# Performance work log

Measured on AMD Instinct MI355X. Metric: run time of the kernel, lower is better.

Reference implementation:

```python
import jax, jax.numpy as jnp
import numpy as np

D, M, K, L, H, BS = 128, 8, 256, 2, 256, 1024


def setup_inputs() -> dict:
    key = jax.random.key(0)
    ks = jax.random.split(key, 7)
    s_d = 1.0 / np.sqrt(D)
    s_2d = 1.0 / np.sqrt(2 * D)
    s_h = 1.0 / np.sqrt(H)
    x = jax.random.normal(ks[0], (BS, D), jnp.float32)
    codebook0 = jax.random.uniform(ks[1], (K, D), jnp.float32, -s_d, s_d)
    codebooks = jax.random.uniform(ks[2], (M - 1, K, D), jnp.float32, -s_d, s_d)
    Wc = jax.random.uniform(ks[3], (M - 1, D, 2 * D), jnp.float32, -s_2d, s_2d)
    bc = jax.random.uniform(ks[4], (M - 1, D), jnp.float32, -s_2d, s_2d)
    W1 = jax.random.uniform(ks[5], (M - 1, L, H, D), jnp.float32, -s_d, s_d)
    W2 = jax.random.uniform(ks[6], (M - 1, L, D, H), jnp.float32, -s_h, s_h)
    return {"x": x, "codebook0": codebook0, "codebooks": codebooks,
            "Wc": Wc, "bc": bc, "W1": W1, "W2": W2}


def _step_targets(xhat, cb, Wc_m, bc_m, W1_m, W2_m):
    """Candidate quantization targets for one step. xhat:[bs,d], cb:[K,d] -> [bs,K,d].
    MLPconcat(concat(zqs, xhat)) is split into the zqs part and the xhat part so the
    [bs*K, 2d] repeat of the torch code is never materialized (same math)."""
    Wz, Wx = Wc_m[:, :D], Wc_m[:, D:]          # Linear(2d,d): y = cc @ W.T + b
    z = cb[None, :, :] + (cb @ Wz.T)[None, :, :] + (xhat @ Wx.T)[:, None, :] + bc_m  # [bs,K,d]
    for l in range(L):
        z = z + jnp.maximum(jnp.einsum('bkd,hd->bkh', z, W1_m[l]), 0.0) @ W2_m[l].T
    return z + xhat[:, None, :]


def _encode(x, codebook0, codebooks, Wc, bc, W1, W2):
    # step 0: plain nearest-centroid assignment (assign_to_codebook)
    d0 = (x * x).sum(-1, keepdims=True) + (codebook0 * codebook0).sum(-1) - 2.0 * x @ codebook0.T
    code0 = jnp.argmin(d0, axis=1)
    xhat = codebook0[code0]
    codes = [code0]
    xn = (x * x).sum(-1, keepdims=True)        # [bs,1]
    for m in range(M - 1):
        z = _step_targets(xhat, codebooks[m], Wc[m], bc[m], W1[m], W2[m])  # [bs,K,d]
        dist = xn + (z * z).sum(-1) - 2.0 * jnp.einsum('bd,bkd->bk', x, z)
        idx = jnp.argmin(dist, axis=1)
        xhat = jnp.take_along_axis(z, idx[:, None, None], axis=1)[:, 0, :]
        codes.append(idx)
    return jnp.stack(codes, axis=1)            # [bs, M] int


def _decode(codes, codebook0, codebooks, Wc, bc, W1, W2):
    xhat = codebook0[codes[:, 0]]
    side = [xhat]
    for m in range(M - 1):
        zq = codebooks[m][codes[:, m + 1]]     # [bs,d]
        Wz, Wx = Wc[m][:, :D], Wc[m][:, D:]
        z = zq + zq @ Wz.T + xhat @ Wx.T + bc[m]
        for l in range(L):
            z = z + jnp.maximum(z @ W1[m, l].T, 0.0) @ W2[m, l].T
        xhat = xhat + z
        side.append(xhat)
    return xhat, side


def reference(x, codebook0, codebooks, Wc, bc, W1, W2):
    # forward(): encode under no_grad, then differentiable decode with side outputs
    codes = jax.lax.stop_gradient(_encode(x, codebook0, codebooks, Wc, bc, W1, W2))
    xhat, side = _decode(codes, codebook0, codebooks, Wc, bc, W1, W2)
    return (xhat, codes, tuple(side))
```

## Files before the change

kernel.cpp:

```cpp
#include <hip/hip_runtime.h>


typedef _Float16 f16;
typedef f16 half4_t __attribute__((ext_vector_type(4)));
typedef f16 half8_t __attribute__((ext_vector_type(8)));
typedef float f32x16 __attribute__((ext_vector_type(16)));

#define OUT_CODES 131072
#define OUT_SIDE  139264

#define WS_XHAT  0
#define WS_RB    131072
#define WS_Y     262144
#define WS_ZC    393216
#define WS_BESTD 425984
#define WS_BESTI 430080
#define WS_BESTZ 434176
#define WS_WSPLIT 960000
#define NW1 458752

#define HLO 8192

__device__ __forceinline__ f32x16 mfma_f16(half8_t a, half8_t b, f32x16 c) {
  return __builtin_amdgcn_mfma_f32_32x32x16_f16(a, b, c, 0, 0, 0);
}

__global__ __launch_bounds__(256) void k_wsplit(const float* __restrict__ W1,
    const float* __restrict__ W2, f16* __restrict__ wsh)
{
  int i = (blockIdx.x * 256 + threadIdx.x) * 4;
  const float* src;
  f16* hi;
  if (i < NW1) { src = W1 + i; hi = wsh + i; }
  else         { src = W2 + (i - NW1); hi = wsh + 2 * NW1 + (i - NW1); }
  f16* lo = hi + NW1;
  float4 v = *(const float4*)src;
  half4_t h, l;
  float s;
  s = v.x * 256.f; h[0] = (f16)s; l[0] = (f16)(s - (float)h[0]);
  s = v.y * 256.f; h[1] = (f16)s; l[1] = (f16)(s - (float)h[1]);
  s = v.z * 256.f; h[2] = (f16)s; l[2] = (f16)(s - (float)h[2]);
  s = v.w * 256.f; h[3] = (f16)s; l[3] = (f16)(s - (float)h[3]);
  *(half4_t*)hi = h;
  *(half4_t*)lo = l;
}

__global__ __launch_bounds__(256) void k_step0(const float* __restrict__ x,
    const float* __restrict__ cb0, float* __restrict__ ws, float* __restrict__ out)
{
  __shared__ float xs[128];
  __shared__ float redv[4];
  __shared__ int   redi[4];
  __shared__ int   kwin;
  int tx = threadIdx.x, b = blockIdx.x;
  if (tx < 128) xs[tx] = x[b * 128 + tx];
  __syncthreads();
  const float* c = cb0 + tx * 128;
  float s = 0.f;
  for (int d = 0; d < 128; d += 4) {
    float4 cv = *(const float4*)(c + d);
    float4 xv = *(const float4*)(xs + d);
    float a0 = xv.x - cv.x, a1 = xv.y - cv.y, a2 = xv.z - cv.z, a3 = xv.w - cv.w;
    s += a0 * a0 + a1 * a1 + a2 * a2 + a3 * a3;
  }
  float v = s; int idx = tx;
  for (int off = 32; off; off >>= 1) {
    float v2 = __shfl_xor(v, off);
    int   i2 = __shfl_xor(idx, off);
    if (v2 < v || (v2 == v && i2 < idx)) { v = v2; idx = i2; }
  }
  if ((tx & 63) == 0) { redv[tx >> 6] = v; redi[tx >> 6] = idx; }
  __syncthreads();
  if (tx == 0) {
    float bv = redv[0]; int bi = redi[0];
    for (int w = 1; w < 4; w++)
      if (redv[w] < bv || (redv[w] == bv && redi[w] < bi)) { bv = redv[w]; bi = redi[w]; }
    kwin = bi;
    out[OUT_CODES + b * 8] = (float)bi;
  }
  __syncthreads();
  int k = kwin;
  if (tx < 128) {
    float xh = cb0[k * 128 + tx];
    ws[WS_XHAT + b * 128 + tx] = xh;
    ws[WS_RB   + b * 128 + tx] = xs[tx] - xh;
    out[OUT_SIDE + b * 128 + tx] = xh;
  }
}

__global__ __launch_bounds__(128) void k_prep(const float* __restrict__ cb,
    const float* __restrict__ Wc, const float* __restrict__ bcm, float* __restrict__ ws)
{
  __shared__ float row[128];
  int tx = threadIdx.x, blk = blockIdx.x;
  if (blk < 256) {
    row[tx] = cb[blk * 128 + tx];
    __syncthreads();
    const float* wrow = Wc + tx * 256;
    float s = 0.f;
    for (int d = 0; d < 128; d += 4) {
      float4 wv = *(const float4*)(wrow + d);
      float4 zv = *(const float4*)(row + d);
      s += wv.x * zv.x + wv.y * zv.y + wv.z * zv.z + wv.w * zv.w;
    }
    ws[WS_ZC + blk * 128 + tx] = row[tx] + s + bcm[tx];
  } else {
    int b = blk - 256;
    row[tx] = ws[WS_XHAT + b * 128 + tx];
    __syncthreads();
    const float* wrow = Wc + tx * 256 + 128;
    float s = 0.f;
    for (int d = 0; d < 128; d += 4) {
      float4 wv = *(const float4*)(wrow + d);
      float4 zv = *(const float4*)(row + d);
      s += wv.x * zv.x + wv.y * zv.y + wv.z * zv.z + wv.w * zv.w;
    }
    ws[WS_Y + b * 128 + tx] = s;
  }
}

__global__ __launch_bounds__(256, 2) void k_step(const f16* __restrict__ wsh,
    float* __restrict__ ws, int sm)
{
  __shared__ __align__(16) f16 lds[32768];
  f16* Zh = lds;
  f16* Zl = lds + HLO;
  f16* Hh = lds + 2 * HLO;
  f16* Hl = lds + 3 * HLO;
  int tx = threadIdx.x;
  int lane = tx & 63, w = tx >> 6;
  int col = lane & 31, koct = lane >> 5;
  int b = blockIdx.x >> 2, t = blockIdx.x & 3, k0 = t << 6;

  {
    const float* zc = ws + WS_ZC + k0 * 128;
    const float* y  = ws + WS_Y + b * 128;
    for (int idx = tx; idx < 1024; idx += 256) {
      int m = idx & 63, d0 = (idx >> 6) << 3;
      float4 a  = *(const float4*)(zc + m * 128 + d0);
      float4 bb = *(const float4*)(zc + m * 128 + d0 + 4);
      float4 ya = *(const float4*)(y + d0);
      float4 yb = *(const float4*)(y + d0 + 4);
      float sv[8] = {a.x + ya.x, a.y + ya.y, a.z + ya.z, a.w + ya.w,
                     bb.x + yb.x, bb.y + yb.y, bb.z + yb.z, bb.w + yb.w};
      half8_t h8, l8;
#pragma unroll
      for (int j = 0; j < 8; j++) {
        float v = sv[j] * 256.f;
        f16 h = (f16)v; h8[j] = h; l8[j] = (f16)(v - (float)h);
      }
      int c0 = (d0 + ((m & 15) << 3)) & 127;
      *(half8_t*)(Zh + (m << 7) + c0) = h8;
      *(half8_t*)(Zl + (m << 7) + c0) = l8;
    }
  }
  __syncthreads();

  const int rot0 = (col & 15) << 3;
  const f16* Zr0 = Zh + (col << 7);
  const f16* Zr1 = Zh + ((col + 32) << 7);
  const f16* Hr0 = Hh + (col << 7);
  const f16* Hr1 = Hh + ((col + 32) << 7);

  for (int l = 0; l < 2; l++) {
    const f16* w1h = wsh + (size_t)((sm * 2 + l) * 256) * 128;
    const f16* w2h = wsh + 2 * NW1 + (size_t)((sm * 2 + l) * 128) * 256;
    f32x16 acc2[2];
#pragma unroll
    for (int i = 0; i < 16; i++) { acc2[0][i] = 0.f; acc2[1][i] = 0.f; }

    half8_t a1hv[8], a1lv[8];
    {
      const f16* a1p = w1h + (size_t)((w << 5) + col) * 128 + (koct << 3);
#pragma unroll
      for (int kc = 0; kc < 8; kc++) {
        a1hv[kc] = *(const half8_t*)(a1p + (kc << 4));
        a1lv[kc] = *(const half8_t*)(a1p + NW1 + (kc << 4));
      }
    }
    f32x16 acc1[2];
#pragma unroll
    for (int i = 0; i < 16; i++) { acc1[0][i] = 0.f; acc1[1][i] = 0.f; }
    __builtin_amdgcn_s_setprio(1);
#pragma unroll
    for (int kc = 0; kc < 8; kc++) {
      int poff = (((kc << 4) + (koct << 3)) + rot0) & 127;
      half8_t bh0 = *(const half8_t*)(Zr0 + poff);
      half8_t bl0 = *(const half8_t*)(Zr0 + HLO + poff);
      half8_t bh1 = *(const half8_t*)(Zr1 + poff);
      half8_t bl1 = *(const half8_t*)(Zr1 + HLO + poff);
      acc1[0] = mfma_f16(a1hv[kc], bh0, acc1[0]);
      acc1[1] = mfma_f16(a1hv[kc], bh1, acc1[1]);
      acc1[0] = mfma_f16(a1lv[kc], bh0, acc1[0]);
      acc1[1] = mfma_f16(a1lv[kc], bh1, acc1[1]);
      acc1[0] = mfma_f16(a1hv[kc], bl0, acc1[0]);
      acc1[1] = mfma_f16(a1hv[kc], bl1, acc1[1]);
    }
    __builtin_amdgcn_s_setprio(0);

    half8_t a2hv[8], a2lv[8];
    {
      const f16* a2p = w2h + (size_t)((w << 5) + col) * 256 + (koct << 3);
#pragma unroll
      for (int kc = 0; kc < 8; kc++) {
        a2hv[kc] = *(const half8_t*)(a2p + (kc << 4));
        a2lv[kc] = *(const half8_t*)(a2p + NW1 + (kc << 4));
      }
    }

#pragma unroll
    for (int mt = 0; mt < 2; mt++) {
      int m = (mt << 5) + col;
#pragma unroll
      for (int qd = 0; qd < 4; qd++) {
        half4_t hv, lv;
#pragma unroll
        for (int j = 0; j < 4; j++) {
          float tv = fmaxf(acc1[mt][(qd << 2) + j], 0.f) * 0.00390625f;
          f16 h = (f16)tv; hv[j] = h; lv[j] = (f16)(tv - (float)h);
        }
        int c = (((w << 5) + (qd << 3) + (koct << 2)) + rot0) & 127;
        *(half4_t*)(Hh + (m << 7) + c) = hv;
        *(half4_t*)(Hl + (m << 7) + c) = lv;
      }
    }
    __syncthreads();

    __builtin_amdgcn_s_setprio(1);
#pragma unroll
    for (int kc = 0; kc < 8; kc++) {
      int poff = (((kc << 4) + (koct << 3)) + rot0) & 127;
      half8_t bh0 = *(const half8_t*)(Hr0 + poff);
      half8_t bl0 = *(const half8_t*)(Hr0 + HLO + poff);
      half8_t bh1 = *(const half8_t*)(Hr1 + poff);
      half8_t bl1 = *(const half8_t*)(Hr1 + HLO + poff);
      acc2[0] = mfma_f16(a2hv[kc], bh0, acc2[0]);
      acc2[1] = mfma_f16(a2hv[kc], bh1, acc2[1]);
      acc2[0] = mfma_f16(a2lv[kc], bh0, acc2[0]);
      acc2[1] = mfma_f16(a2lv[kc], bh1, acc2[1]);
      acc2[0] = mfma_f16(a2hv[kc], bl0, acc2[0]);
      acc2[1] = mfma_f16(a2hv[kc], bl1, acc2[1]);
    }
    __builtin_amdgcn_s_setprio(0);

    {
      const f16* a1p = w1h + (size_t)(128 + (w << 5) + col) * 128 + (koct << 3);
#pragma unroll
      for (int kc = 0; kc < 8; kc++) {
        a1hv[kc] = *(const half8_t*)(a1p + (kc << 4));
        a1lv[kc] = *(const half8_t*)(a1p + NW1 + (kc << 4));
      }
    }
#pragma unroll
    for (int i = 0; i < 16; i++) { acc1[0][i] = 0.f; acc1[1][i] = 0.f; }
    __builtin_amdgcn_s_setprio(1);
#pragma unroll
    for (int kc = 0; kc < 8; kc++) {
      int poff = (((kc << 4) + (koct << 3)) + rot0) & 127;
      half8_t bh0 = *(const half8_t*)(Zr0 + poff);
      half8_t bl0 = *(const half8_t*)(Zr0 + HLO + poff);
      half8_t bh1 = *(const half8_t*)(Zr1 + poff);
      half8_t bl1 = *(const half8_t*)(Zr1 + HLO + poff);
      acc1[0] = mfma_f16(a1hv[kc], bh0, acc1[0]);
      acc1[1] = mfma_f16(a1hv[kc], bh1, acc1[1]);
      acc1[0] = mfma_f16(a1lv[kc], bh0, acc1[0]);
      acc1[1] = mfma_f16(a1lv[kc], bh1, acc1[1]);
      acc1[0] = mfma_f16(a1hv[kc], bl0, acc1[0]);
      acc1[1] = mfma_f16(a1hv[kc], bl1, acc1[1]);
    }
    __builtin_amdgcn_s_setprio(0);

    {
      const f16* a2q = w2h + (size_t)((w << 5) + col) * 256 + 128 + (koct << 3);
#pragma unroll
      for (int kc = 0; kc < 8; kc++) {
        a2hv[kc] = *(const half8_t*)(a2q + (kc << 4));
        a2lv[kc] = *(const half8_t*)(a2q + NW1 + (kc << 4));
      }
    }
    __syncthreads();

#pragma unroll
    for (int mt = 0; mt < 2; mt++) {
      int m = (mt << 5) + col;
#pragma unroll
      for (int qd = 0; qd < 4; qd++) {
        half4_t hv, lv;
#pragma unroll
        for (int j = 0; j < 4; j++) {
          float tv = fmaxf(acc1[mt][(qd << 2) + j], 0.f) * 0.00390625f;
          f16 h = (f16)tv; hv[j] = h; lv[j] = (f16)(tv - (float)h);
        }
        int c = (((w << 5) + (qd << 3) + (koct << 2)) + rot0) & 127;
        *(half4_t*)(Hh + (m << 7) + c) = hv;
        *(half4_t*)(Hl + (m << 7) + c) = lv;
      }
    }
    __syncthreads();

    __builtin_amdgcn_s_setprio(1);
#pragma unroll
    for (int kc = 0; kc < 8; kc++) {
      int poff = (((kc << 4) + (koct << 3)) + rot0) & 127;
      half8_t bh0 = *(const half8_t*)(Hr0 + poff);
      half8_t bl0 = *(const half8_t*)(Hr0 + HLO + poff);
      half8_t bh1 = *(const half8_t*)(Hr1 + poff);
      half8_t bl1 = *(const half8_t*)(Hr1 + HLO + poff);
      acc2[0] = mfma_f16(a2hv[kc], bh0, acc2[0]);
      acc2[1] = mfma_f16(a2hv[kc], bh1, acc2[1]);
      acc2[0] = mfma_f16(a2lv[kc], bh0, acc2[0]);
      acc2[1] = mfma_f16(a2lv[kc], bh1, acc2[1]);
      acc2[0] = mfma_f16(a2hv[kc], bl0, acc2[0]);
      acc2[1] = mfma_f16(a2hv[kc], bl1, acc2[1]);
    }
    __builtin_amdgcn_s_setprio(0);

#pragma unroll
    for (int mt = 0; mt < 2; mt++) {
      int m = (mt << 5) + col;
      f16* zhr = Zh + (m << 7);
      f16* zlr = Zl + (m << 7);
#pragma unroll
      for (int qd = 0; qd < 4; qd++) {
        int c = (((w << 5) + (qd << 3) + (koct << 2)) + rot0) & 127;
        half4_t zh = *(half4_t*)(zhr + c);
        half4_t zl = *(half4_t*)(zlr + c);
#pragma unroll
        for (int j = 0; j < 4; j++) {
          float zs = (float)zh[j] + (float)zl[j];
          zs += acc2[mt][(qd << 2) + j] * 0.00390625f;
          f16 h = (f16)zs; zh[j] = h; zl[j] = (f16)(zs - (float)h);
        }
        *(half4_t*)(zhr + c) = zh;
        *(half4_t*)(zlr + c) = zl;
      }
    }
    __syncthreads();
  }

  float* pd = (float*)Hh;
  int* rwin = (int*)Hh + 64;
  {
    int row = tx >> 2, seg = tx & 3;
    int rotr = (row & 15) << 3;
    const f16* zhr = Zh + (row << 7);
    const f16* zlr = Zl + (row << 7);
    const float* rb = ws + WS_RB + b * 128 + (seg << 5);
    float s = 0.f;
#pragma unroll
    for (int o = 0; o < 4; o++) {
      int c = (((seg << 5) + (o << 3)) + rotr) & 127;
      half8_t zh = *(const half8_t*)(zhr + c);
      half8_t zl = *(const half8_t*)(zlr + c);
      float4 r0 = *(const float4*)(rb + (o << 3));
      float4 r1 = *(const float4*)(rb + (o << 3) + 4);
      float rr[8] = {r0.x, r0.y, r0.z, r0.w, r1.x, r1.y, r1.z, r1.w};
#pragma unroll
      for (int j = 0; j < 8; j++) {
        float z = ((float)zh[j] + (float)zl[j]) * 0.00390625f;
        float dlt = rr[j] - z;
        s += dlt * dlt;
      }
    }
    s += __shfl_xor(s, 1);
    s += __shfl_xor(s, 2);
    if (seg == 0) pd[row] = s;
  }
  __syncthreads();
  if (tx < 64) {
    float v = pd[tx]; int idx = tx;
#pragma unroll
    for (int off = 32; off; off >>= 1) {
      float v2 = __shfl_xor(v, off);
      int   i2 = __shfl_xor(idx, off);
      if (v2 < v || (v2 == v && i2 < idx)) { v = v2; idx = i2; }
    }
    if (tx == 0) {
      ws[WS_BESTD + (b << 2) + t] = v;
      ((int*)ws)[WS_BESTI + (b << 2) + t] = k0 + idx;
      rwin[0] = idx;
    }
  }
  __syncthreads();
  if (tx < 32) {
    int rw = rwin[0];
    int c = ((tx << 2) + ((rw & 15) << 3)) & 127;
    half4_t zh = *(const half4_t*)(Zh + (rw << 7) + c);
    half4_t zl = *(const half4_t*)(Zl + (rw << 7) + c);
    float4 z;
    z.x = ((float)zh[0] + (float)zl[0]) * 0.00390625f;
    z.y = ((float)zh[1] + (float)zl[1]) * 0.00390625f;
    z.z = ((float)zh[2] + (float)zl[2]) * 0.00390625f;
    z.w = ((float)zh[3] + (float)zl[3]) * 0.00390625f;
    *(float4*)(ws + WS_BESTZ + (((b << 2) + t) << 7) + (tx << 2)) = z;
  }
}

__global__ __launch_bounds__(128) void k_update(const float* __restrict__ x,
    float* __restrict__ ws, float* __restrict__ out, int m, int last)
{
  __shared__ int tsel;
  int tx = threadIdx.x, b = blockIdx.x;
  if (tx == 0) {
    float bv = ws[WS_BESTD + (b << 2)]; int bt = 0;
    for (int q = 1; q < 4; q++) {
      float v = ws[WS_BESTD + (b << 2) + q];
      if (v < bv) { bv = v; bt = q; }
    }
    tsel = bt;
    int k = ((const int*)ws)[WS_BESTI + (b << 2) + bt];
    out[OUT_CODES + b * 8 + (m + 1)] = (float)k;
  }
  __syncthreads();
  int bt = tsel;
  float z  = ws[WS_BESTZ + (((b << 2) + bt) << 7) + tx];
  float xh = ws[WS_XHAT + b * 128 + tx] + z;
  ws[WS_XHAT + b * 128 + tx] = xh;
  ws[WS_RB   + b * 128 + tx] = x[b * 128 + tx] - xh;
  out[OUT_SIDE + (m + 1) * 131072 + b * 128 + tx] = xh;
  if (last) out[b * 128 + tx] = xh;
}

extern "C" void kernel_launch(void* const* d_in, const int* in_sizes, int n_in,
                              void* d_out, int out_size, void* d_ws, size_t ws_size,
                              hipStream_t stream)
{
  const float* x   = (const float*)d_in[0];
  const float* cb0 = (const float*)d_in[1];
  const float* cbs = (const float*)d_in[2];
  const float* Wc  = (const float*)d_in[3];
  const float* bc  = (const float*)d_in[4];
  const float* W1  = (const float*)d_in[5];
  const float* W2  = (const float*)d_in[6];
  float* out = (float*)d_out;
  float* ws  = (float*)d_ws;
  f16* wsh = (f16*)(ws + WS_WSPLIT);

  k_wsplit<<<896, 256, 0, stream>>>(W1, W2, wsh);
  k_step0<<<1024, 256, 0, stream>>>(x, cb0, ws, out);
  for (int m = 0; m < 7; m++) {
    k_prep<<<1280, 128, 0, stream>>>(cbs + m * 256 * 128, Wc + m * 128 * 256,
                                     bc + m * 128, ws);
    k_step<<<4096, 256, 0, stream>>>(wsh, ws, m);
    k_update<<<1024, 128, 0, stream>>>(x, ws, out, m, (m == 6) ? 1 : 0);
  }
}
```

Before: 2.160 ms.

## Process 64-candidate tile as two 32-row subtiles to halve LDS and raise occupancy

Each k_step block now handles its 64 codebook candidates in two sequential passes of 32, so the LDS Z/H buffers shrink to half and accumulators drop from two f32x16 to one. Launch bounds move from 2 to 4 blocks per SIMD-group so more waves can be resident. In exchange, W1/W2 weight fragments are reloaded from global/L2 for each subtile and there are twice as many barriers, with a running best kept across subtiles.

```diff
diff --git a/kernel.cpp b/kernel.cpp
--- a/kernel.cpp
+++ b/kernel.cpp
@@ -19,7 +19,7 @@
 #define WS_WSPLIT 960000
 #define NW1 458752
 
-#define HLO 8192
+#define HLO 4096
 
 __device__ __forceinline__ f32x16 mfma_f16(half8_t a, half8_t b, f32x16 c) {
   return __builtin_amdgcn_mfma_f32_32x32x16_f16(a, b, c, 0, 0, 0);
@@ -119,10 +119,10 @@
   }
 }
 
-__global__ __launch_bounds__(256, 2) void k_step(const f16* __restrict__ wsh,
+__global__ __launch_bounds__(256, 4) void k_step(const f16* __restrict__ wsh,
     float* __restrict__ ws, int sm)
 {
-  __shared__ __align__(16) f16 lds[32768];
+  __shared__ __align__(16) f16 lds[16384];
   f16* Zh = lds;
   f16* Zl = lds + HLO;
   f16* Hh = lds + 2 * HLO;
@@ -132,267 +132,248 @@
   int col = lane & 31, koct = lane >> 5;
   int b = blockIdx.x >> 2, t = blockIdx.x & 3, k0 = t << 6;
 
-  {
-    const float* zc = ws + WS_ZC + k0 * 128;
-    const float* y  = ws + WS_Y + b * 128;
-    for (int idx = tx; idx < 1024; idx += 256) {
-      int m = idx & 63, d0 = (idx >> 6) << 3;
-      float4 a  = *(const float4*)(zc + m * 128 + d0);
-      float4 bb = *(const float4*)(zc + m * 128 + d0 + 4);
-      float4 ya = *(const float4*)(y + d0);
-      float4 yb = *(const float4*)(y + d0 + 4);
-      float sv[8] = {a.x + ya.x, a.y + ya.y, a.z + ya.z, a.w + ya.w,
-                     bb.x + yb.x, bb.y + yb.y, bb.z + yb.z, bb.w + yb.w};
-      half8_t h8, l8;
-#pragma unroll
-      for (int j = 0; j < 8; j++) {
-        float v = sv[j] * 256.f;
-        f16 h = (f16)v; h8[j] = h; l8[j] = (f16)(v - (float)h);
-      }
-      int c0 = (d0 + ((m & 15) << 3)) & 127;
-      *(half8_t*)(Zh + (m << 7) + c0) = h8;
-      *(half8_t*)(Zl + (m << 7) + c0) = l8;
-    }
-  }
-  __syncthreads();
-
   const int rot0 = (col & 15) << 3;
   const f16* Zr0 = Zh + (col << 7);
-  const f16* Zr1 = Zh + ((col + 32) << 7);
   const f16* Hr0 = Hh + (col << 7);
-  const f16* Hr1 = Hh + ((col + 32) << 7);
-
-  for (int l = 0; l < 2; l++) {
-    const f16* w1h = wsh + (size_t)((sm * 2 + l) * 256) * 128;
-    const f16* w2h = wsh + 2 * NW1 + (size_t)((sm * 2 + l) * 128) * 256;
-    f32x16 acc2[2];
-#pragma unroll
-    for (int i = 0; i < 16; i++) { acc2[0][i] = 0.f; acc2[1][i] = 0.f; }
-
-    half8_t a1hv[8], a1lv[8];
+  float* pd = (float*)Hh;
+  int* rwin = (int*)Hh + 64;
+
+  float bestd = 3.4e38f;
+  int   besti = 0;
+
+  for (int st = 0; st < 2; st++) {
+    int kb = k0 + (st << 5);
+
     {
-      const f16* a1p = w1h + (size_t)((w << 5) + col) * 128 + (koct << 3);
+      const float* zc = ws + WS_ZC + kb * 128;
+      const float* y  = ws + WS_Y + b * 128;
+      for (int idx = tx; idx < 512; idx += 256) {
+        int m = idx & 31, d0 = (idx >> 5) << 3;
+        float4 a  = *(const float4*)(zc + m * 128 + d0);
+        float4 bb = *(const float4*)(zc + m * 128 + d0 + 4);
+        float4 ya = *(const float4*)(y + d0);
+        float4 yb = *(const float4*)(y + d0 + 4);
+        float sv[8] = {a.x + ya.x, a.y + ya.y, a.z + ya.z, a.w + ya.w,
+                       bb.x + yb.x, bb.y + yb.y, bb.z + yb.z, bb.w + yb.w};
+        half8_t h8, l8;
+#pragma unroll
+        for (int j = 0; j < 8; j++) {
+          float v = sv[j] * 256.f;
+          f16 h = (f16)v; h8[j] = h; l8[j] = (f16)(v - (float)h);
+        }
+        int c0 = (d0 + ((m & 15) << 3)) & 127;
+        *(half8_t*)(Zh + (m << 7) + c0) = h8;
+        *(half8_t*)(Zl + (m << 7) + c0) = l8;
+      }
+    }
+    __syncthreads();
+
+    for (int l = 0; l < 2; l++) {
+      const f16* w1h = wsh + (size_t)((sm * 2 + l) * 256) * 128;
+      const f16* w2h = wsh + 2 * NW1 + (size_t)((sm * 2 + l) * 128) * 256;
+      f32x16 acc2;
+#pragma unroll
+      for (int i = 0; i < 16; i++) acc2[i] = 0.f;
+
+      half8_t a1hv[8], a1lv[8];
+      {
+        const f16* a1p = w1h + (size_t)((w << 5) + col) * 128 + (koct << 3);
+#pragma unroll
+        for (int kc = 0; kc < 8; kc++) {
+          a1hv[kc] = *(const half8_t*)(a1p + (kc << 4));
+          a1lv[kc] = *(const half8_t*)(a1p + NW1 + (kc << 4));
+        }
+      }
+      f32x16 acc1;
+#pragma unroll
+      for (int i = 0; i < 16; i++) acc1[i] = 0.f;
+      __builtin_amdgcn_s_setprio(1);
 #pragma unroll
       for (int kc = 0; kc < 8; kc++) {
-        a1hv[kc] = *(const half8_t*)(a1p + (kc << 4));
-        a1lv[kc] = *(const half8_t*)(a1p + NW1 + (kc << 4));
-      }
-    }
-    f32x16 acc1[2];
-#pragma unroll
-    for (int i = 0; i < 16; i++) { acc1[0][i] = 0.f; acc1[1][i] = 0.f; }
-    __builtin_amdgcn_s_setprio(1);
-#pragma unroll
-    for (int kc = 0; kc < 8; kc++) {
-      int poff = (((kc << 4) + (koct << 3)) + rot0) & 127;
-      half8_t bh0 = *(const half8_t*)(Zr0 + poff);
-      half8_t bl0 = *(const half8_t*)(Zr0 + HLO + poff);
-      half8_t bh1 = *(const half8_t*)(Zr1 + poff);
-      half8_t bl1 = *(const half8_t*)(Zr1 + HLO + poff);
-      acc1[0] = mfma_f16(a1hv[kc], bh0, acc1[0]);
-      acc1[1] = mfma_f16(a1hv[kc], bh1, acc1[1]);
-      acc1[0] = mfma_f16(a1lv[kc], bh0, acc1[0]);
-      acc1[1] = mfma_f16(a1lv[kc], bh1, acc1[1]);
-      acc1[0] = mfma_f16(a1hv[kc], bl0, acc1[0]);
-      acc1[1] = mfma_f16(a1hv[kc], bl1, acc1[1]);
-    }
-    __builtin_amdgcn_s_setprio(0);
-
-    half8_t a2hv[8], a2lv[8];
-    {
-      const f16* a2p = w2h + (size_t)((w << 5) + col) * 256 + (koct << 3);
-#pragma unroll
-      for (int kc = 0; kc < 8; kc++) {
-        a2hv[kc] = *(const half8_t*)(a2p + (kc << 4));
-        a2lv[kc] = *(const half8_t*)(a2p + NW1 + (kc << 4));
-      }
-    }
-
-#pragma unroll
-    for (int mt = 0; mt < 2; mt++) {
-      int m = (mt << 5) + col;
+        int poff = (((kc << 4) + (koct << 3)) + rot0) & 127;
+        half8_t bh0 = *(const half8_t*)(Zr0 + poff);
+        half8_t bl0 = *(const half8_t*)(Zr0 + HLO + poff);
+        acc1 = mfma_f16(a1hv[kc], bh0, acc1);
+        acc1 = mfma_f16(a1lv[kc], bh0, acc1);
+        acc1 = mfma_f16(a1hv[kc], bl0, acc1);
+      }
+      __builtin_amdgcn_s_setprio(0);
+
+      half8_t a2hv[8], a2lv[8];
+      {
+        const f16* a2p = w2h + (size_t)((w << 5) + col) * 256 + (koct << 3);
+#pragma unroll
+        for (int kc = 0; kc < 8; kc++) {
+          a2hv[kc] = *(const half8_t*)(a2p + (kc << 4));
+          a2lv[kc] = *(const half8_t*)(a2p + NW1 + (kc << 4));
+        }
+      }
+
 #pragma unroll
       for (int qd = 0; qd < 4; qd++) {
         half4_t hv, lv;
 #pragma unroll
         for (int j = 0; j < 4; j++) {
-          float tv = fmaxf(acc1[mt][(qd << 2) + j], 0.f) * 0.00390625f;
+          float tv = fmaxf(acc1[(qd << 2) + j], 0.f) * 0.00390625f;
           f16 h = (f16)tv; hv[j] = h; lv[j] = (f16)(tv - (float)h);
         }
         int c = (((w << 5) + (qd << 3) + (koct << 2)) + rot0) & 127;
-        *(half4_t*)(Hh + (m << 7) + c) = hv;
-        *(half4_t*)(Hl + (m << 7) + c) = lv;
-      }
-    }
-    __syncthreads();
-
-    __builtin_amdgcn_s_setprio(1);
-#pragma unroll
-    for (int kc = 0; kc < 8; kc++) {
-      int poff = (((kc << 4) + (koct << 3)) + rot0) & 127;
-      half8_t bh0 = *(const half8_t*)(Hr0 + poff);
-      half8_t bl0 = *(const half8_t*)(Hr0 + HLO + poff);
-      half8_t bh1 = *(const half8_t*)(Hr1 + poff);
-      half8_t bl1 = *(const half8_t*)(Hr1 + HLO + poff);
-      acc2[0] = mfma_f16(a2hv[kc], bh0, acc2[0]);
-      acc2[1] = mfma_f16(a2hv[kc], bh1, acc2[1]);
-      acc2[0] = mfma_f16(a2lv[kc], bh0, acc2[0]);
-      acc2[1] = mfma_f16(a2lv[kc], bh1, acc2[1]);
-      acc2[0] = mfma_f16(a2hv[kc], bl0, acc2[0]);
-      acc2[1] = mfma_f16(a2hv[kc], bl1, acc2[1]);
-    }
-    __builtin_amdgcn_s_setprio(0);
-
-    {
-      const f16* a1p = w1h + (size_t)(128 + (w << 5) + col) * 128 + (koct << 3);
+        *(half4_t*)(Hh + (col << 7) + c) = hv;
+        *(half4_t*)(Hl + (col << 7) + c) = lv;
+      }
+      __syncthreads();
+
+      __builtin_amdgcn_s_setprio(1);
 #pragma unroll
       for (int kc = 0; kc < 8; kc++) {
-        a1hv[kc] = *(const half8_t*)(a1p + (kc << 4));
-        a1lv[kc] = *(const half8_t*)(a1p + NW1 + (kc << 4));
-      }
-    }
-#pragma unroll
-    for (int i = 0; i < 16; i++) { acc1[0][i] = 0.f; acc1[1][i] = 0.f; }
-    __builtin_amdgcn_s_setprio(1);
-#pragma unroll
-    for (int kc = 0; kc < 8; kc++) {
-      int poff = (((kc << 4) + (koct << 3)) + rot0) & 127;
-      half8_t bh0 = *(const half8_t*)(Zr0 + poff);
-      half8_t bl0 = *(const half8_t*)(Zr0 + HLO + poff);
-      half8_t bh1 = *(const half8_t*)(Zr1 + poff);
-      half8_t bl1 = *(const half8_t*)(Zr1 + HLO + poff);
-      acc1[0] = mfma_f16(a1hv[kc], bh0, acc1[0]);
-      acc1[1] = mfma_f16(a1hv[kc], bh1, acc1[1]);
-      acc1[0] = mfma_f16(a1lv[kc], bh0, acc1[0]);
-      acc1[1] = mfma_f16(a1lv[kc], bh1, acc1[1]);
-      acc1[0] = mfma_f16(a1hv[kc], bl0, acc1[0]);
-      acc1[1] = mfma_f16(a1hv[kc], bl1, acc1[1]);
-    }
-    __builtin_amdgcn_s_setprio(0);
-
-    {
-      const f16* a2q = w2h + (size_t)((w << 5) + col) * 256 + 128 + (koct << 3);
+        int poff = (((kc << 4) + (koct << 3)) + rot0) & 127;
+        half8_t bh0 = *(const half8_t*)(Hr0 + poff);
+        half8_t bl0 = *(const half8_t*)(Hr0 + HLO + poff);
+        acc2 = mfma_f16(a2hv[kc], bh0, acc2);
+        acc2 = mfma_f16(a2lv[kc], bh0, acc2);
+        acc2 = mfma_f16(a2hv[kc], bl0, acc2);
+      }
+      __builtin_amdgcn_s_setprio(0);
+
+      {
+        const f16* a1p = w1h + (size_t)(128 + (w << 5) + col) * 128 + (koct << 3);
+#pragma unroll
+        for (int kc = 0; kc < 8; kc++) {
+          a1hv[kc] = *(const half8_t*)(a1p + (kc << 4));
+          a1lv[kc] = *(const half8_t*)(a1p + NW1 + (kc << 4));
+        }
+      }
+#pragma unroll
+      for (int i = 0; i < 16; i++) acc1[i] = 0.f;
+      __builtin_amdgcn_s_setprio(1);
 #pragma unroll
       for (int kc = 0; kc < 8; kc++) {
-        a2hv[kc] = *(const half8_t*)(a2q + (kc << 4));
-        a2lv[kc] = *(const half8_t*)(a2q + NW1 + (kc << 4));
-      }
-    }
-    __syncthreads();
-
-#pragma unroll
-    for (int mt = 0; mt < 2; mt++) {
-      int m = (mt << 5) + col;
+        int poff = (((kc << 4) + (koct << 3)) + rot0) & 127;
+        half8_t bh0 = *(const half8_t*)(Zr0 + poff);
+        half8_t bl0 = *(const half8_t*)(Zr0 + HLO + poff);
+        acc1 = mfma_f16(a1hv[kc], bh0, acc1);
+        acc1 = mfma_f16(a1lv[kc], bh0, acc1);
+        acc1 = mfma_f16(a1hv[kc], bl0, acc1);
+      }
+      __builtin_amdgcn_s_setprio(0);
+
+      {
+        const f16* a2q = w2h + (size_t)((w << 5) + col) * 256 + 128 + (koct << 3);
+#pragma unroll
+        for (int kc = 0; kc < 8; kc++) {
+          a2hv[kc] = *(const half8_t*)(a2q + (kc << 4));
+          a2lv[kc] = *(const half8_t*)(a2q + NW1 + (kc << 4));
+        }
+      }
+      __syncthreads();
+
 #pragma unroll
       for (int qd = 0; qd < 4; qd++) {
         half4_t hv, lv;
 #pragma unroll
         for (int j = 0; j < 4; j++) {
-          float tv = fmaxf(acc1[mt][(qd << 2) + j], 0.f) * 0.00390625f;
+          float tv = fmaxf(acc1[(qd << 2) + j], 0.f) * 0.00390625f;
           f16 h = (f16)tv; hv[j] = h; lv[j] = (f16)(tv - (float)h);
         }
         int c = (((w << 5) + (qd << 3) + (koct << 2)) + rot0) & 127;
-        *(half4_t*)(Hh + (m << 7) + c) = hv;
-        *(half4_t*)(Hl + (m << 7) + c) = lv;
-      }
-    }
-    __syncthreads();
-
-    __builtin_amdgcn_s_setprio(1);
-#pragma unroll
-    for (int kc = 0; kc < 8; kc++) {
-      int poff = (((kc << 4) + (koct << 3)) + rot0) & 127;
-      half8_t bh0 = *(const half8_t*)(Hr0 + poff);
-      half8_t bl0 = *(const half8_t*)(Hr0 + HLO + poff);
-      half8_t bh1 = *(const half8_t*)(Hr1 + poff);
-      half8_t bl1 = *(const half8_t*)(Hr1 + HLO + poff);
-      acc2[0] = mfma_f16(a2hv[kc], bh0, acc2[0]);
-      acc2[1] = mfma_f16(a2hv[kc], bh1, acc2[1]);
-      acc2[0] = mfma_f16(a2lv[kc], bh0, acc2[0]);
-      acc2[1] = mfma_f16(a2lv[kc], bh1, acc2[1]);
-      acc2[0] = mfma_f16(a2hv[kc], bl0, acc2[0]);
-      acc2[1] = mfma_f16(a2hv[kc], bl1, acc2[1]);
-    }
-    __builtin_amdgcn_s_setprio(0);
-
-#pragma unroll
-    for (int mt = 0; mt < 2; mt++) {
-      int m = (mt << 5) + col;
-      f16* zhr = Zh + (m << 7);
-      f16* zlr = Zl + (m << 7);
-#pragma unroll
-      for (int qd = 0; qd < 4; qd++) {
-        int c = (((w << 5) + (qd << 3) + (koct << 2)) + rot0) & 127;
-        half4_t zh = *(half4_t*)(zhr + c);
-        half4_t zl = *(half4_t*)(zlr + c);
-#pragma unroll
-        for (int j = 0; j < 4; j++) {
-          float zs = (float)zh[j] + (float)zl[j];
-          zs += acc2[mt][(qd << 2) + j] * 0.00390625f;
-          f16 h = (f16)zs; zh[j] = h; zl[j] = (f16)(zs - (float)h);
-        }
-        *(half4_t*)(zhr + c) = zh;
-        *(half4_t*)(zlr + c) = zl;
-      }
-    }
-    __syncthreads();
-  }
-
-  float* pd = (float*)Hh;
-  int* rwin = (int*)Hh + 64;
-  {
-    int row = tx >> 2, seg = tx & 3;
-    int rotr = (row & 15) << 3;
-    const f16* zhr = Zh + (row << 7);
-    const f16* zlr = Zl + (row << 7);
-    const float* rb = ws + WS_RB + b * 128 + (seg << 5);
-    float s = 0.f;
-#pragma unroll
-    for (int o = 0; o < 4; o++) {
-      int c = (((seg << 5) + (o << 3)) + rotr) & 127;
-      half8_t zh = *(const half8_t*)(zhr + c);
-      half8_t zl = *(const half8_t*)(zlr + c);
-      float4 r0 = *(const float4*)(rb + (o << 3));
-      float4 r1 = *(const float4*)(rb + (o << 3) + 4);
-      float rr[8] = {r0.x, r0.y, r0.z, r0.w, r1.x, r1.y, r1.z, r1.w};
-#pragma unroll
-      for (int j = 0; j < 8; j++) {
-        float z = ((float)zh[j] + (float)zl[j]) * 0.00390625f;
-        float dlt = rr[j] - z;
-        s += dlt * dlt;
-      }
-    }
-    s += __shfl_xor(s, 1);
-    s += __shfl_xor(s, 2);
-    if (seg == 0) pd[row] = s;
-  }
-  __syncthreads();
-  if (tx < 64) {
-    float v = pd[tx]; int idx = tx;
-#pragma unroll
-    for (int off = 32; off; off >>= 1) {
-      float v2 = __shfl_xor(v, off);
-      int   i2 = __shfl_xor(idx, off);
-      if (v2 < v || (v2 == v && i2 < idx)) { v = v2; idx = i2; }
-    }
-    if (tx == 0) {
-      ws[WS_BESTD + (b << 2) + t] = v;
-      ((int*)ws)[WS_BESTI + (b << 2) + t] = k0 + idx;
-      rwin[0] = idx;
-    }
-  }
-  __syncthreads();
-  if (tx < 32) {
-    int rw = rwin[0];
-    int c = ((tx << 2) + ((rw & 15) << 3)) & 127;
-    half4_t zh = *(const half4_t*)(Zh + (rw << 7) + c);
-    half4_t zl = *(const half4_t*)(Zl + (rw << 7) + c);
-    float4 z;
-    z.x = ((float)zh[0] + (float)zl[0]) * 0.00390625f;
-    z.y = ((float)zh[1] + (float)zl[1]) * 0.00390625f;
-    z.z = ((float)zh[2] + (float)zl[2]) * 0.00390625f;
-    z.w = ((float)zh[3] + (float)zl[3]) * 0.00390625f;
-    *(float4*)(ws + WS_BESTZ + (((b << 2) + t) << 7) + (tx << 2)) = z;
+        *(half4_t*)(Hh + (col << 7) + c) = hv;
+        *(half4_t*)(Hl + (col << 7) + c) = lv;
+      }
+      __syncthreads();
+
+      __builtin_amdgcn_s_setprio(1);
+#pragma unroll
+      for (int kc = 0; kc < 8; kc++) {
+        int poff = (((kc << 4) + (koct << 3)) + rot0) & 127;
+        half8_t bh0 = *(const half8_t*)(Hr0 + poff);
+        half8_t bl0 = *(const half8_t*)(Hr0 + HLO + poff);
+        acc2 = mfma_f16(a2hv[kc], bh0, acc2);
+        acc2 = mfma_f16(a2lv[kc], bh0, acc2);
+        acc2 = mfma_f16(a2hv[kc], bl0, acc2);
+      }
+      __builtin_amdgcn_s_setprio(0);
+
+      {
+        f16* zhr = Zh + (col << 7);
+        f16* zlr = Zl + (col << 7);
+#pragma unroll
+        for (int qd = 0; qd < 4; qd++) {
+          int c = (((w << 5) + (qd << 3) + (koct << 2)) + rot0) & 127;
+          half4_t zh = *(half4_t*)(zhr + c);
+          half4_t zl = *(half4_t*)(zlr + c);
+#pragma unroll
+          for (int j = 0; j < 4; j++) {
+            float zs = (float)zh[j] + (float)zl[j];
+            zs += acc2[(qd << 2) + j] * 0.00390625f;
+            f16 h = (f16)zs; zh[j] = h; zl[j] = (f16)(zs - (float)h);
+          }
+          *(half4_t*)(zhr + c) = zh;
+          *(half4_t*)(zlr + c) = zl;
+        }
+      }
+      __syncthreads();
+    }
+
+    if (tx < 128) {
+      int row = tx >> 2, seg = tx & 3;
+      int rotr = (row & 15) << 3;
+      const f16* zhr = Zh + (row << 7);
+      const f16* zlr = Zl + (row << 7);
+      const float* rb = ws + WS_RB + b * 128 + (seg << 5);
+      float s = 0.f;
+#pragma unroll
+      for (int o = 0; o < 4; o++) {
+        int c = (((seg << 5) + (o << 3)) + rotr) & 127;
+        half8_t zh = *(const half8_t*)(zhr + c);
+        half8_t zl = *(const half8_t*)(zlr + c);
+        float4 r0 = *(const float4*)(rb + (o << 3));
+        float4 r1 = *(const float4*)(rb + (o << 3) + 4);
+        float rr[8] = {r0.x, r0.y, r0.z, r0.w, r1.x, r1.y, r1.z, r1.w};
+#pragma unroll
+        for (int j = 0; j < 8; j++) {
+          float z = ((float)zh[j] + (float)zl[j]) * 0.00390625f;
+          float dlt = rr[j] - z;
+          s += dlt * dlt;
+        }
+      }
+      s += __shfl_xor(s, 1);
+      s += __shfl_xor(s, 2);
+      if (seg == 0) pd[row] = s;
+    }
+    __syncthreads();
+    if (tx < 32) {
+      float v = pd[tx]; int idx = tx;
+#pragma unroll
+      for (int off = 16; off; off >>= 1) {
+        float v2 = __shfl_xor(v, off);
+        int   i2 = __shfl_xor(idx, off);
+        if (v2 < v || (v2 == v && i2 < idx)) { v = v2; idx = i2; }
+      }
+      if (tx == 0) {
+        int better = (v < bestd) ? 1 : 0;
+        if (better) { bestd = v; besti = kb + idx; rwin[0] = idx; }
+        rwin[1] = better;
+      }
+    }
+    __syncthreads();
+    if (rwin[1] && tx < 32) {
+      int rw = rwin[0];
+      int c = ((tx << 2) + ((rw & 15) << 3)) & 127;
+      half4_t zh = *(const half4_t*)(Zh + (rw << 7) + c);
+      half4_t zl = *(const half4_t*)(Zl + (rw << 7) + c);
+      float4 z;
+      z.x = ((float)zh[0] + (float)zl[0]) * 0.00390625f;
+      z.y = ((float)zh[1] + (float)zl[1]) * 0.00390625f;
+      z.z = ((float)zh[2] + (float)zl[2]) * 0.00390625f;
+      z.w = ((float)zh[3] + (float)zl[3]) * 0.00390625f;
+      *(float4*)(ws + WS_BESTZ + (((b << 2) + t) << 7) + (tx << 2)) = z;
+    }
+    __syncthreads();
+  }
+
+  if (tx == 0) {
+    ws[WS_BESTD + (b << 2) + t] = bestd;
+    ((int*)ws)[WS_BESTI + (b << 2) + t] = besti;
   }
 }
 
```

After: 3.763 ms. +74.2%, slower.
